# Optimization experiments

Hardware: AMD Instinct MI355X
Metric: run time of the kernel (lower is better)

The kernel has to match this reference:

```python
import jax, jax.numpy as jnp
import numpy as np

B, S, E, H, Dh = 1, 2048, 1024, 16, 64


def setup_inputs() -> dict:
    key = jax.random.key(0)
    ks = jax.random.split(key, 9)
    sc = 0.02
    return {
        "x": jax.random.normal(ks[0], (B, S, E), jnp.float32),
        "Wq": jax.random.normal(ks[1], (H, E, Dh), jnp.float32) * sc,
        "bq": jax.random.normal(ks[2], (H, Dh), jnp.float32) * sc,
        "Wk": jax.random.normal(ks[3], (H, E, Dh), jnp.float32) * sc,
        "bk": jax.random.normal(ks[4], (H, Dh), jnp.float32) * sc,
        "Wv": jax.random.normal(ks[5], (H, E, Dh), jnp.float32) * sc,
        "bv": jax.random.normal(ks[6], (H, Dh), jnp.float32) * sc,
        "Wo": jax.random.normal(ks[7], (E, E), jnp.float32) * sc,
        "bo": jax.random.normal(ks[8], (E,), jnp.float32) * sc,
    }


def reference(x, Wq, bq, Wk, bk, Wv, bv, Wo, bo):
    # Per-head projections (stacked): [B,S,E] x [H,E,Dh] -> [B,H,S,Dh]
    q = jnp.einsum("bse,hed->bhsd", x, Wq) + bq[None, :, None, :]
    k = jnp.einsum("bse,hed->bhsd", x, Wk) + bk[None, :, None, :]
    v = jnp.einsum("bse,hed->bhsd", x, Wv) + bv[None, :, None, :]
    scores = jnp.einsum("bhsd,bhtd->bhst", q, k) / np.sqrt(Dh).astype(np.float32)
    causal = jnp.tril(jnp.ones((S, S), dtype=bool))  # [S,S]
    scores = jnp.where(causal[None, None], scores, -jnp.inf)
    attn = jax.nn.softmax(scores, axis=-1)  # attn_dropout p=0 -> identity
    out = jnp.einsum("bhst,bhtd->bhsd", attn, v)
    # concat heads in head order: [B,S,H*Dh]
    out = out.transpose(0, 2, 1, 3).reshape(B, S, H * Dh)
    return out @ Wo.T if False else jnp.einsum("bsf,ef->bse", out, Wo.T.T * 0 + Wo) if False else out @ Wo.swapaxes(0, 1) * 0 + (jnp.einsum("bsf,fe->bse", out, Wo) + bo)
```

## Files before the change

kernel.cpp:

```cpp
#include <hip/hip_runtime.h>
#include <hip/hip_bf16.h>

#define S_LEN 2048
#define E_DIM 1024
#define NH 16
#define DH 64

typedef __bf16 v8bf __attribute__((ext_vector_type(8)));
typedef __bf16 v4bf __attribute__((ext_vector_type(4)));
typedef float f32x4 __attribute__((ext_vector_type(4)));
typedef unsigned short u16x4 __attribute__((ext_vector_type(4)));
typedef unsigned short u16x8 __attribute__((ext_vector_type(8)));

__device__ __align__(16) unsigned short g_Xb[S_LEN * E_DIM];
__device__ __align__(16) unsigned short g_WT[3 * E_DIM * E_DIM];
__device__ __align__(16) unsigned short g_WoT[E_DIM * E_DIM];
__device__ __align__(16) unsigned short g_Qb[NH * S_LEN * DH];
__device__ __align__(16) unsigned short g_Kb[NH * S_LEN * DH];
__device__ __align__(16) unsigned short g_Vt[NH * DH * S_LEN];
__device__ __align__(16) unsigned short g_AO[S_LEN * E_DIM];

__device__ inline unsigned short f2bf(float f) {
    unsigned int u = __float_as_uint(f);
    u += 0x7FFF + ((u >> 16) & 1);
    return (unsigned short)(u >> 16);
}
__device__ inline f32x4 mfma16(v8bf a, v8bf b, f32x4 c) {
    return __builtin_amdgcn_mfma_f32_16x16x32_bf16(a, b, c, 0, 0, 0);
}
__device__ inline f32x4 mfma16k16(v4bf a, v4bf b, f32x4 c) {
#if __has_builtin(__builtin_amdgcn_mfma_f32_16x16x16_bf16)
    return __builtin_amdgcn_mfma_f32_16x16x16_bf16(a, b, c, 0, 0, 0);
#elif __has_builtin(__builtin_amdgcn_mfma_f32_16x16x16bf16_1k)
    typedef short s4v __attribute__((ext_vector_type(4)));
    union UA { v4bf v; s4v s; };
    UA ua, ub; ua.v = a; ub.v = b;
    return __builtin_amdgcn_mfma_f32_16x16x16bf16_1k(ua.s, ub.s, c, 0, 0, 0);
#else
    asm("v_mfma_f32_16x16x16_bf16 %0, %1, %2, %0" : "+v"(c) : "v"(a), "v"(b));
    return c;
#endif
}

typedef __attribute__((address_space(3))) unsigned int lds_u32;
typedef __attribute__((address_space(1))) const unsigned int glb_u32;
__device__ inline void async_cp16(const unsigned short* g, unsigned short* l) {
    __builtin_amdgcn_global_load_lds((glb_u32*)g, (lds_u32*)l, 16, 0, 0);
}

__global__ __launch_bounds__(256) void prep(const float* __restrict__ X,
                                            const float* __restrict__ Wq,
                                            const float* __restrict__ Wk,
                                            const float* __restrict__ Wv,
                                            const float* __restrict__ Wo) {
    __shared__ __align__(16) unsigned short lds[64 * 72];
    const int b = blockIdx.x;
    const int t = threadIdx.x;
    if (b < 2048) {
        int i = b * 256 + t;
        f32x4 v = reinterpret_cast<const f32x4*>(X)[i];
        u16x4 o = {f2bf(v.x), f2bf(v.y), f2bf(v.z), f2bf(v.w)};
        reinterpret_cast<u16x4*>(g_Xb)[i] = o;
    } else if (b < 2304) {
        int bb = b - 2048;
        const int h = bb >> 4;
        const int e0 = (bb & 15) * 64;
        const float* srcs[3] = {Wq, Wk, Wv};
#pragma unroll
        for (int tn = 0; tn < 3; tn++) {
            const float* W = srcs[tn] + h * 65536;
#pragma unroll
            for (int p = 0; p < 4; p++) {
                int e = p * 16 + (t >> 4);
                int d = (t & 15) * 4;
                f32x4 v = *reinterpret_cast<const f32x4*>(&W[(e0 + e) * 64 + d]);
                lds[(d + 0) * 72 + e] = f2bf(v.x);
                lds[(d + 1) * 72 + e] = f2bf(v.y);
                lds[(d + 2) * 72 + e] = f2bf(v.z);
                lds[(d + 3) * 72 + e] = f2bf(v.w);
            }
            __syncthreads();
#pragma unroll
            for (int p = 0; p < 2; p++) {
                int d = p * 32 + (t >> 3);
                int ec = (t & 7) * 8;
                u16x8 o = *reinterpret_cast<const u16x8*>(&lds[d * 72 + ec]);
                *reinterpret_cast<u16x8*>(&g_WT[(tn * 1024 + h * 64 + d) * E_DIM + e0 + ec]) = o;
            }
            __syncthreads();
        }
    } else {
        int bb = b - 2304;
        const int f0 = (bb >> 4) * 64;
        const int e0 = (bb & 15) * 64;
#pragma unroll
        for (int p = 0; p < 4; p++) {
            int f = p * 16 + (t >> 4);
            int e = (t & 15) * 4;
            f32x4 v = *reinterpret_cast<const f32x4*>(&Wo[(f0 + f) * E_DIM + e0 + e]);
            lds[(e + 0) * 72 + f] = f2bf(v.x);
            lds[(e + 1) * 72 + f] = f2bf(v.y);
            lds[(e + 2) * 72 + f] = f2bf(v.z);
            lds[(e + 3) * 72 + f] = f2bf(v.w);
        }
        __syncthreads();
#pragma unroll
        for (int p = 0; p < 2; p++) {
            int e = p * 32 + (t >> 3);
            int fc = (t & 7) * 8;
            u16x8 o = *reinterpret_cast<const u16x8*>(&lds[e * 72 + fc]);
            *reinterpret_cast<u16x8*>(&g_WoT[(e0 + e) * E_DIM + f0 + fc]) = o;
        }
    }
}

__global__ __launch_bounds__(256) void qkv_gemm(const float* __restrict__ bq,
                                                const float* __restrict__ bk,
                                                const float* __restrict__ bv) {
    __shared__ __align__(16) unsigned short lds[24576];
    const int t = threadIdx.x;
    const int wave = t >> 6;
    const int lane = t & 63;
    const int m = lane & 15, quad = lane >> 4;
    const int s0 = blockIdx.x * 128;
    const int n0 = blockIdx.y * 64;

    const int rl = t >> 3;
    const int cx = (t & 7) ^ (rl & 7);
    const int axor = m & 7;

    f32x4 acc[2][4];
#pragma unroll
    for (int i = 0; i < 2; i++)
#pragma unroll
        for (int j = 0; j < 4; j++) acc[i][j] = (f32x4){0.f, 0.f, 0.f, 0.f};

    const unsigned short* gA = g_Xb + (s0 + rl) * E_DIM + cx * 8;
    const unsigned short* gB = g_WT + (n0 + rl) * E_DIM + cx * 8;

    auto stage = [&](int k0, int buf) {
        unsigned short* lA = lds + buf * 12288;
        unsigned short* lB = lA + 8192;
        const unsigned short* ga = gA + k0;
        async_cp16(ga,              lA + wave * 512);
        async_cp16(ga + 32 * E_DIM, lA + 2048 + wave * 512);
        async_cp16(ga + 64 * E_DIM, lA + 4096 + wave * 512);
        async_cp16(ga + 96 * E_DIM, lA + 6144 + wave * 512);
        const unsigned short* gb = gB + k0;
        async_cp16(gb,              lB + wave * 512);
        async_cp16(gb + 32 * E_DIM, lB + 2048 + wave * 512);
    };

    stage(0, 0);
    __syncthreads();
    int buf = 0;
    for (int k0 = 0; k0 < E_DIM; k0 += 64) {
        if (k0 + 64 < E_DIM) stage(k0 + 64, buf ^ 1);
        const unsigned short* lA = lds + buf * 12288;
        const unsigned short* lB = lA + 8192;
        const unsigned short* lAr0 = lA + (wave * 32 + m) * 64;
        const unsigned short* lAr1 = lAr0 + 16 * 64;
#pragma unroll
        for (int ks = 0; ks < 2; ks++) {
            const int ch = ((ks * 4 + quad) ^ axor) * 8;
            v8bf a0 = *reinterpret_cast<const v8bf*>(lAr0 + ch);
            v8bf a1 = *reinterpret_cast<const v8bf*>(lAr1 + ch);
#pragma unroll
            for (int j = 0; j < 4; j++) {
                v8bf bfr = *reinterpret_cast<const v8bf*>(lB + (j * 16 + m) * 64 + ch);
                acc[0][j] = mfma16(a0, bfr, acc[0][j]);
                acc[1][j] = mfma16(a1, bfr, acc[1][j]);
            }
        }
        __syncthreads();
        buf ^= 1;
    }

    const int tensor = n0 >> 10;
    const int nn0 = n0 & 1023;
    const int hh = nn0 >> 6;
    const float* bb = tensor == 0 ? bq : (tensor == 1 ? bk : bv);
    float bias[4];
#pragma unroll
    for (int j = 0; j < 4; j++) bias[j] = bb[nn0 + j * 16 + m];

    if (tensor < 2) {
#pragma unroll
        for (int i = 0; i < 2; i++)
#pragma unroll
            for (int j = 0; j < 4; j++)
#pragma unroll
                for (int r = 0; r < 4; r++) {
                    int sl = wave * 32 + i * 16 + quad * 4 + r;
                    int nl = j * 16 + m;
                    lds[sl * 72 + nl] = f2bf(acc[i][j][r] + bias[j]);
                }
        __syncthreads();
        unsigned short* dst = (tensor == 0 ? g_Qb : g_Kb) + (hh * S_LEN + s0) * DH;
#pragma unroll
        for (int p = 0; p < 4; p++) {
            int row = p * 32 + (t >> 3);
            int c = t & 7;
            u16x8 v = *reinterpret_cast<const u16x8*>(&lds[row * 72 + c * 8]);
            *reinterpret_cast<u16x8*>(&dst[row * DH + c * 8]) = v;
        }
    } else {
#pragma unroll
        for (int i = 0; i < 2; i++)
#pragma unroll
            for (int j = 0; j < 4; j++)
#pragma unroll
                for (int r = 0; r < 4; r++) {
                    int sl = wave * 32 + i * 16 + quad * 4 + r;
                    int nl = j * 16 + m;
                    lds[nl * 136 + sl] = f2bf(acc[i][j][r] + bias[j]);
                }
        __syncthreads();
#pragma unroll
        for (int p = 0; p < 4; p++) {
            int nl = p * 16 + (t >> 4);
            int sc = t & 15;
            u16x8 v = *reinterpret_cast<const u16x8*>(&lds[nl * 136 + sc * 8]);
            *reinterpret_cast<u16x8*>(&g_Vt[(hh * DH + nl) * S_LEN + s0 + sc * 8]) = v;
        }
    }
}

__global__ __launch_bounds__(256) void flash_attn() {
    __shared__ __align__(16) float comb[256 * 20];
    const int t = threadIdx.x;
    const int wave = t >> 6, lane = t & 63;
    const int m = lane & 15, quad = lane >> 4;
    const int h = blockIdx.x & 15;
    const int Tp = blockIdx.x >> 4;
    const int qq = Tp >> 4, tt = Tp & 15;
    const int T = (qq == 0) ? 63 - tt : (qq == 1) ? 32 + tt : (qq == 2) ? 31 - tt : tt;
    const int s0 = T * 32;

    const unsigned short* Qh = g_Qb + h * S_LEN * DH;
    const unsigned short* Kh = g_Kb + h * S_LEN * DH;
    const unsigned short* Vh = g_Vt + h * DH * S_LEN;

    v8bf aqA0 = *reinterpret_cast<const v8bf*>(Qh + (s0 + m) * DH + quad * 8);
    v8bf aqA1 = *reinterpret_cast<const v8bf*>(Qh + (s0 + m) * DH + 32 + quad * 8);
    v8bf aqB0 = *reinterpret_cast<const v8bf*>(Qh + (s0 + 16 + m) * DH + quad * 8);
    v8bf aqB1 = *reinterpret_cast<const v8bf*>(Qh + (s0 + 16 + m) * DH + 32 + quad * 8);

    f32x4 oA[4], oB[4];
#pragma unroll
    for (int i = 0; i < 4; i++) { oA[i] = (f32x4){0.f,0.f,0.f,0.f}; oB[i] = (f32x4){0.f,0.f,0.f,0.f}; }
    float lA = 0.f, lB = 0.f;

    const float SC = 0.125f * 1.44269504088896f;
    const int tEnd = s0 + 32;
    const int tq = quad * 4;

    int t0 = wave * 64;
    v8bf kf[4][2];
    v4bf vf[4][4];
    if (t0 < tEnd) {
#pragma unroll
        for (int ct = 0; ct < 4; ct++) {
            const unsigned short* kp = Kh + (t0 + ct * 16 + m) * DH + quad * 8;
            kf[ct][0] = *reinterpret_cast<const v8bf*>(kp);
            kf[ct][1] = *reinterpret_cast<const v8bf*>(kp + 32);
        }
#pragma unroll
        for (int dt = 0; dt < 4; dt++)
#pragma unroll
            for (int ct = 0; ct < 4; ct++)
                vf[dt][ct] = *reinterpret_cast<const v4bf*>(Vh + (dt * 16 + m) * S_LEN + t0 + ct * 16 + tq);
    }

    for (; t0 < tEnd; t0 += 256) {
        const int t1 = t0 + 256;
        const bool doA = (t0 <= s0 + 15);

        f32x4 sB[4], sA[4];
        __builtin_amdgcn_s_setprio(1);
#pragma unroll
        for (int ct = 0; ct < 4; ct++) {
            if (t0 + ct * 16 <= s0 + 31) {
                sB[ct] = (f32x4){0.f,0.f,0.f,0.f};
                sB[ct] = mfma16(kf[ct][0], aqB0, sB[ct]);
                sB[ct] = mfma16(kf[ct][1], aqB1, sB[ct]);
            }
        }
        if (doA) {
#pragma unroll
            for (int ct = 0; ct < 4; ct++) {
                if (t0 + ct * 16 <= s0 + 15) {
                    sA[ct] = (f32x4){0.f,0.f,0.f,0.f};
                    sA[ct] = mfma16(kf[ct][0], aqA0, sA[ct]);
                    sA[ct] = mfma16(kf[ct][1], aqA1, sA[ct]);
                }
            }
        }
        __builtin_amdgcn_s_setprio(0);

        if (t1 < tEnd) {
#pragma unroll
            for (int ct = 0; ct < 4; ct++) {
                const unsigned short* kp = Kh + (t1 + ct * 16 + m) * DH + quad * 8;
                kf[ct][0] = *reinterpret_cast<const v8bf*>(kp);
                kf[ct][1] = *reinterpret_cast<const v8bf*>(kp + 32);
            }
        }

        v4bf ptB[4];
#pragma unroll
        for (int ct = 0; ct < 4; ct++) {
            if (t0 + ct * 16 <= s0 + 31) {
                const int tb = t0 + ct * 16 + tq;
                if (t0 + ct * 16 + 15 > s0 + 16) {
#pragma unroll
                    for (int r = 0; r < 4; r++)
                        if (tb + r > s0 + 16 + m) sB[ct][r] = -3e38f;
                }
#pragma unroll
                for (int r = 0; r < 4; r++)
                    sB[ct][r] = __builtin_amdgcn_exp2f(sB[ct][r] * SC);
                lB += sB[ct][0] + sB[ct][1] + sB[ct][2] + sB[ct][3];
                __hip_bfloat162 b01 = __float22bfloat162_rn(make_float2(sB[ct][0], sB[ct][1]));
                __hip_bfloat162 b23 = __float22bfloat162_rn(make_float2(sB[ct][2], sB[ct][3]));
                union { unsigned int u[2]; v4bf v; } pk;
                pk.u[0] = *reinterpret_cast<unsigned int*>(&b01);
                pk.u[1] = *reinterpret_cast<unsigned int*>(&b23);
                ptB[ct] = pk.v;
            }
        }
        __builtin_amdgcn_s_setprio(1);
#pragma unroll
        for (int ct = 0; ct < 4; ct++) {
            if (t0 + ct * 16 <= s0 + 31) {
#pragma unroll
                for (int dt = 0; dt < 4; dt++)
                    oB[dt] = mfma16k16(vf[dt][ct], ptB[ct], oB[dt]);
            }
        }
        __builtin_amdgcn_s_setprio(0);

        if (doA) {
            v4bf ptA[4];
#pragma unroll
            for (int ct = 0; ct < 4; ct++) {
                if (t0 + ct * 16 <= s0 + 15) {
                    const int tb = t0 + ct * 16 + tq;
                    if (t0 + ct * 16 + 15 > s0) {
#pragma unroll
                        for (int r = 0; r < 4; r++)
                            if (tb + r > s0 + m) sA[ct][r] = -3e38f;
                    }
#pragma unroll
                    for (int r = 0; r < 4; r++)
                        sA[ct][r] = __builtin_amdgcn_exp2f(sA[ct][r] * SC);
                    lA += sA[ct][0] + sA[ct][1] + sA[ct][2] + sA[ct][3];
                    __hip_bfloat162 b01 = __float22bfloat162_rn(make_float2(sA[ct][0], sA[ct][1]));
                    __hip_bfloat162 b23 = __float22bfloat162_rn(make_float2(sA[ct][2], sA[ct][3]));
                    union { unsigned int u[2]; v4bf v; } pk;
                    pk.u[0] = *reinterpret_cast<unsigned int*>(&b01);
                    pk.u[1] = *reinterpret_cast<unsigned int*>(&b23);
                    ptA[ct] = pk.v;
                }
            }
            __builtin_amdgcn_s_setprio(1);
#pragma unroll
            for (int ct = 0; ct < 4; ct++) {
                if (t0 + ct * 16 <= s0 + 15) {
#pragma unroll
                    for (int dt = 0; dt < 4; dt++)
                        oA[dt] = mfma16k16(vf[dt][ct], ptA[ct], oA[dt]);
                }
            }
            __builtin_amdgcn_s_setprio(0);
        }

        if (t1 < tEnd) {
#pragma unroll
            for (int dt = 0; dt < 4; dt++)
#pragma unroll
                for (int ct = 0; ct < 4; ct++)
                    vf[dt][ct] = *reinterpret_cast<const v4bf*>(Vh + (dt * 16 + m) * S_LEN + t1 + ct * 16 + tq);
        }
    }

    float* cw = comb + t * 20;
#pragma unroll
    for (int dt = 0; dt < 4; dt++) *reinterpret_cast<f32x4*>(cw + dt * 4) = oA[dt];
    cw[16] = lA;
    __syncthreads();
    {
        f32x4 os = (f32x4){0.f,0.f,0.f,0.f};
        float ls = 0.f;
#pragma unroll
        for (int w = 0; w < 4; w++) {
            const float* cr = comb + (w * 64 + lane) * 20;
            os += *reinterpret_cast<const f32x4*>(cr + wave * 4);
#pragma unroll
            for (int q2 = 0; q2 < 4; q2++)
                ls += comb[(w * 64 + q2 * 16 + m) * 20 + 16];
        }
        float inv = 1.0f / ls;
        u16x4 ov = {f2bf(os[0] * inv), f2bf(os[1] * inv), f2bf(os[2] * inv), f2bf(os[3] * inv)};
        *reinterpret_cast<u16x4*>(&g_AO[(s0 + m) * E_DIM + h * 64 + wave * 16 + quad * 4]) = ov;
    }
    __syncthreads();
#pragma unroll
    for (int dt = 0; dt < 4; dt++) *reinterpret_cast<f32x4*>(cw + dt * 4) = oB[dt];
    cw[16] = lB;
    __syncthreads();
    {
        f32x4 os = (f32x4){0.f,0.f,0.f,0.f};
        float ls = 0.f;
#pragma unroll
        for (int w = 0; w < 4; w++) {
            const float* cr = comb + (w * 64 + lane) * 20;
            os += *reinterpret_cast<const f32x4*>(cr + wave * 4);
#pragma unroll
            for (int q2 = 0; q2 < 4; q2++)
                ls += comb[(w * 64 + q2 * 16 + m) * 20 + 16];
        }
        float inv = 1.0f / ls;
        u16x4 ov = {f2bf(os[0] * inv), f2bf(os[1] * inv), f2bf(os[2] * inv), f2bf(os[3] * inv)};
        *reinterpret_cast<u16x4*>(&g_AO[(s0 + 16 + m) * E_DIM + h * 64 + wave * 16 + quad * 4]) = ov;
    }
}

__global__ __launch_bounds__(256) void out_gemm(const float* __restrict__ bo,
                                                float* __restrict__ OUT) {
    __shared__ __align__(16) unsigned short lds[24576];
    const int t = threadIdx.x;
    const int wave = t >> 6;
    const int lane = t & 63;
    const int m = lane & 15, quad = lane >> 4;
    const int s0 = blockIdx.x * 128;
    const int n0 = blockIdx.y * 64;

    const int rl = t >> 3;
    const int cx = (t & 7) ^ (rl & 7);
    const int axor = m & 7;

    f32x4 acc[2][4];
#pragma unroll
    for (int i = 0; i < 2; i++)
#pragma unroll
        for (int j = 0; j < 4; j++) acc[i][j] = (f32x4){0.f, 0.f, 0.f, 0.f};

    const unsigned short* gA = g_AO + (s0 + rl) * E_DIM + cx * 8;
    const unsigned short* gB = g_WoT + (n0 + rl) * E_DIM + cx * 8;

    auto stage = [&](int k0, int buf) {
        unsigned short* lA = lds + buf * 12288;
        unsigned short* lB = lA + 8192;
        const unsigned short* ga = gA + k0;
        async_cp16(ga,              lA + wave * 512);
        async_cp16(ga + 32 * E_DIM, lA + 2048 + wave * 512);
        async_cp16(ga + 64 * E_DIM, lA + 4096 + wave * 512);
        async_cp16(ga + 96 * E_DIM, lA + 6144 + wave * 512);
        const unsigned short* gb = gB + k0;
        async_cp16(gb,              lB + wave * 512);
        async_cp16(gb + 32 * E_DIM, lB + 2048 + wave * 512);
    };

    stage(0, 0);
    __syncthreads();
    int buf = 0;
    for (int k0 = 0; k0 < E_DIM; k0 += 64) {
        if (k0 + 64 < E_DIM) stage(k0 + 64, buf ^ 1);
        const unsigned short* lA = lds + buf * 12288;
        const unsigned short* lB = lA + 8192;
        const unsigned short* lAr0 = lA + (wave * 32 + m) * 64;
        const unsigned short* lAr1 = lAr0 + 16 * 64;
#pragma unroll
        for (int ks = 0; ks < 2; ks++) {
            const int ch = ((ks * 4 + quad) ^ axor) * 8;
            v8bf a0 = *reinterpret_cast<const v8bf*>(lAr0 + ch);
            v8bf a1 = *reinterpret_cast<const v8bf*>(lAr1 + ch);
#pragma unroll
            for (int j = 0; j < 4; j++) {
                v8bf bfr = *reinterpret_cast<const v8bf*>(lB + (j * 16 + m) * 64 + ch);
                acc[0][j] = mfma16(a0, bfr, acc[0][j]);
                acc[1][j] = mfma16(a1, bfr, acc[1][j]);
            }
        }
        __syncthreads();
        buf ^= 1;
    }
#pragma unroll
    for (int i = 0; i < 2; i++)
#pragma unroll
        for (int j = 0; j < 4; j++) {
            int e = n0 + j * 16 + m;
            float bias = bo[e];
#pragma unroll
            for (int r = 0; r < 4; r++) {
                int s = s0 + wave * 32 + i * 16 + quad * 4 + r;
                OUT[s * E_DIM + e] = acc[i][j][r] + bias;
            }
        }
}

extern "C" void kernel_launch(void* const* d_in, const int* in_sizes, int n_in,
                              void* d_out, int out_size, void* d_ws, size_t ws_size,
                              hipStream_t stream) {
    (void)in_sizes; (void)n_in; (void)out_size; (void)d_ws; (void)ws_size;
    const float* x  = (const float*)d_in[0];
    const float* Wq = (const float*)d_in[1];
    const float* bq = (const float*)d_in[2];
    const float* Wk = (const float*)d_in[3];
    const float* bk = (const float*)d_in[4];
    const float* Wv = (const float*)d_in[5];
    const float* bv = (const float*)d_in[6];
    const float* Wo = (const float*)d_in[7];
    const float* bo = (const float*)d_in[8];
    float* out = (float*)d_out;

    hipLaunchKernelGGL(prep,       dim3(2560),   dim3(256), 0, stream, x, Wq, Wk, Wv, Wo);
    hipLaunchKernelGGL(qkv_gemm,   dim3(16, 48), dim3(256), 0, stream, bq, bk, bv);
    hipLaunchKernelGGL(flash_attn, dim3(1024),   dim3(256), 0, stream);
    hipLaunchKernelGGL(out_gemm,   dim3(16, 16), dim3(256), 0, stream, bo, out);
}
```

Measured before the change: 184.9 us.

## Store K and V in MFMA-fragment tiled layout for contiguous attention loads

The projection epilogue now writes K and V into a tiled layout that matches the MFMA fragment order, 16-key blocks of 1024 elements. Each wave's K and V fragment loads in the flash-attention kernel become contiguous offsets instead of strided row reads, which matters most for the transposed V loads that used to stride by the full sequence length. The per-column-tile causal bounds checks are removed, so some fully masked tiles are now computed and zeroed by the mask. The block-to-query-tile order is also reversed, so light tiles are now scheduled before heavy ones, which may worsen tail balance.

```diff
diff --git a/kernel.cpp b/kernel.cpp
--- a/kernel.cpp
+++ b/kernel.cpp
@@ -196,13 +196,26 @@
                     lds[sl * 72 + nl] = f2bf(acc[i][j][r] + bias[j]);
                 }
         __syncthreads();
-        unsigned short* dst = (tensor == 0 ? g_Qb : g_Kb) + (hh * S_LEN + s0) * DH;
-#pragma unroll
-        for (int p = 0; p < 4; p++) {
-            int row = p * 32 + (t >> 3);
-            int c = t & 7;
-            u16x8 v = *reinterpret_cast<const u16x8*>(&lds[row * 72 + c * 8]);
-            *reinterpret_cast<u16x8*>(&dst[row * DH + c * 8]) = v;
+        if (tensor == 0) {
+            unsigned short* dst = g_Qb + (hh * S_LEN + s0) * DH;
+#pragma unroll
+            for (int p = 0; p < 4; p++) {
+                int row = p * 32 + (t >> 3);
+                int c = t & 7;
+                u16x8 v = *reinterpret_cast<const u16x8*>(&lds[row * 72 + c * 8]);
+                *reinterpret_cast<u16x8*>(&dst[row * DH + c * 8]) = v;
+            }
+        } else {
+            unsigned short* dst = g_Kb + hh * S_LEN * DH;
+            const int tb0 = s0 >> 4;
+#pragma unroll
+            for (int p = 0; p < 4; p++) {
+                int row = p * 32 + (t >> 3);
+                int c = t & 7;
+                u16x8 v = *reinterpret_cast<const u16x8*>(&lds[row * 72 + c * 8]);
+                int idx = (tb0 + (row >> 4)) * 1024 + (c >> 2) * 512 + (row & 15) * 32 + (c & 3) * 8;
+                *reinterpret_cast<u16x8*>(&dst[idx]) = v;
+            }
         }
     } else {
 #pragma unroll
@@ -216,12 +229,14 @@
                     lds[nl * 136 + sl] = f2bf(acc[i][j][r] + bias[j]);
                 }
         __syncthreads();
+        unsigned short* dst = g_Vt + hh * S_LEN * DH;
 #pragma unroll
         for (int p = 0; p < 4; p++) {
             int nl = p * 16 + (t >> 4);
             int sc = t & 15;
             u16x8 v = *reinterpret_cast<const u16x8*>(&lds[nl * 136 + sc * 8]);
-            *reinterpret_cast<u16x8*>(&g_Vt[(hh * DH + nl) * S_LEN + s0 + sc * 8]) = v;
+            int idx = ((s0 >> 4) + (sc >> 1)) * 1024 + (nl >> 4) * 256 + (nl & 15) * 16 + (sc & 1) * 8;
+            *reinterpret_cast<u16x8*>(&dst[idx]) = v;
         }
     }
 }
@@ -234,12 +249,15 @@
     const int h = blockIdx.x & 15;
     const int Tp = blockIdx.x >> 4;
     const int qq = Tp >> 4, tt = Tp & 15;
-    const int T = (qq == 0) ? 63 - tt : (qq == 1) ? 32 + tt : (qq == 2) ? 31 - tt : tt;
+    const int T = (qq == 0) ? tt : (qq == 1) ? 31 - tt : (qq == 2) ? 32 + tt : 63 - tt;
     const int s0 = T * 32;
 
     const unsigned short* Qh = g_Qb + h * S_LEN * DH;
     const unsigned short* Kh = g_Kb + h * S_LEN * DH;
-    const unsigned short* Vh = g_Vt + h * DH * S_LEN;
+    const unsigned short* Vh = g_Vt + h * S_LEN * DH;
+    const int ko = m * 32 + quad * 8;
+    const int vo = m * 16 + quad * 4;
+    const int tq = quad * 4;
 
     v8bf aqA0 = *reinterpret_cast<const v8bf*>(Qh + (s0 + m) * DH + quad * 8);
     v8bf aqA1 = *reinterpret_cast<const v8bf*>(Qh + (s0 + m) * DH + 32 + quad * 8);
@@ -253,134 +271,123 @@
 
     const float SC = 0.125f * 1.44269504088896f;
     const int tEnd = s0 + 32;
-    const int tq = quad * 4;
 
     int t0 = wave * 64;
     v8bf kf[4][2];
     v4bf vf[4][4];
     if (t0 < tEnd) {
+        const unsigned short* kb = Kh + t0 * 64 + ko;
 #pragma unroll
         for (int ct = 0; ct < 4; ct++) {
-            const unsigned short* kp = Kh + (t0 + ct * 16 + m) * DH + quad * 8;
-            kf[ct][0] = *reinterpret_cast<const v8bf*>(kp);
-            kf[ct][1] = *reinterpret_cast<const v8bf*>(kp + 32);
-        }
+            kf[ct][0] = *reinterpret_cast<const v8bf*>(kb + ct * 1024);
+            kf[ct][1] = *reinterpret_cast<const v8bf*>(kb + ct * 1024 + 512);
+        }
+        const unsigned short* vb = Vh + t0 * 64 + vo;
 #pragma unroll
         for (int dt = 0; dt < 4; dt++)
 #pragma unroll
             for (int ct = 0; ct < 4; ct++)
-                vf[dt][ct] = *reinterpret_cast<const v4bf*>(Vh + (dt * 16 + m) * S_LEN + t0 + ct * 16 + tq);
+                vf[dt][ct] = *reinterpret_cast<const v4bf*>(vb + ct * 1024 + dt * 256);
     }
 
     for (; t0 < tEnd; t0 += 256) {
+        const bool doA = (t0 < s0 + 16);
         const int t1 = t0 + 256;
-        const bool doA = (t0 <= s0 + 15);
-
-        f32x4 sB[4], sA[4];
+
         __builtin_amdgcn_s_setprio(1);
+        f32x4 sB[4];
 #pragma unroll
         for (int ct = 0; ct < 4; ct++) {
-            if (t0 + ct * 16 <= s0 + 31) {
-                sB[ct] = (f32x4){0.f,0.f,0.f,0.f};
-                sB[ct] = mfma16(kf[ct][0], aqB0, sB[ct]);
-                sB[ct] = mfma16(kf[ct][1], aqB1, sB[ct]);
-            }
-        }
+            sB[ct] = (f32x4){0.f,0.f,0.f,0.f};
+            sB[ct] = mfma16(kf[ct][0], aqB0, sB[ct]);
+            sB[ct] = mfma16(kf[ct][1], aqB1, sB[ct]);
+        }
+        __builtin_amdgcn_s_setprio(0);
+        v4bf ptB[4];
+#pragma unroll
+        for (int ct = 0; ct < 4; ct++) {
+            const int tb = t0 + ct * 16 + tq;
+            if (t0 + ct * 16 + 15 > s0 + 16) {
+#pragma unroll
+                for (int r = 0; r < 4; r++)
+                    if (tb + r > s0 + 16 + m) sB[ct][r] = -3e38f;
+            }
+#pragma unroll
+            for (int r = 0; r < 4; r++)
+                sB[ct][r] = __builtin_amdgcn_exp2f(sB[ct][r] * SC);
+            lB += sB[ct][0] + sB[ct][1] + sB[ct][2] + sB[ct][3];
+            __hip_bfloat162 b01 = __float22bfloat162_rn(make_float2(sB[ct][0], sB[ct][1]));
+            __hip_bfloat162 b23 = __float22bfloat162_rn(make_float2(sB[ct][2], sB[ct][3]));
+            union { unsigned int u[2]; v4bf v; } pk;
+            pk.u[0] = *reinterpret_cast<unsigned int*>(&b01);
+            pk.u[1] = *reinterpret_cast<unsigned int*>(&b23);
+            ptB[ct] = pk.v;
+        }
+        __builtin_amdgcn_s_setprio(1);
+#pragma unroll
+        for (int dt = 0; dt < 4; dt++)
+#pragma unroll
+            for (int ct = 0; ct < 4; ct++)
+                oB[dt] = mfma16k16(vf[dt][ct], ptB[ct], oB[dt]);
+        __builtin_amdgcn_s_setprio(0);
+
+        f32x4 sA[4];
         if (doA) {
+            __builtin_amdgcn_s_setprio(1);
 #pragma unroll
             for (int ct = 0; ct < 4; ct++) {
-                if (t0 + ct * 16 <= s0 + 15) {
-                    sA[ct] = (f32x4){0.f,0.f,0.f,0.f};
-                    sA[ct] = mfma16(kf[ct][0], aqA0, sA[ct]);
-                    sA[ct] = mfma16(kf[ct][1], aqA1, sA[ct]);
+                sA[ct] = (f32x4){0.f,0.f,0.f,0.f};
+                sA[ct] = mfma16(kf[ct][0], aqA0, sA[ct]);
+                sA[ct] = mfma16(kf[ct][1], aqA1, sA[ct]);
+            }
+            __builtin_amdgcn_s_setprio(0);
+        }
+        if (t1 < tEnd) {
+            const unsigned short* kb = Kh + t1 * 64 + ko;
+#pragma unroll
+            for (int ct = 0; ct < 4; ct++) {
+                kf[ct][0] = *reinterpret_cast<const v8bf*>(kb + ct * 1024);
+                kf[ct][1] = *reinterpret_cast<const v8bf*>(kb + ct * 1024 + 512);
+            }
+        }
+
+        if (doA) {
+            v4bf ptA[4];
+#pragma unroll
+            for (int ct = 0; ct < 4; ct++) {
+                const int tb = t0 + ct * 16 + tq;
+                if (t0 + ct * 16 + 15 > s0) {
+#pragma unroll
+                    for (int r = 0; r < 4; r++)
+                        if (tb + r > s0 + m) sA[ct][r] = -3e38f;
                 }
-            }
-        }
-        __builtin_amdgcn_s_setprio(0);
-
-        if (t1 < tEnd) {
-#pragma unroll
-            for (int ct = 0; ct < 4; ct++) {
-                const unsigned short* kp = Kh + (t1 + ct * 16 + m) * DH + quad * 8;
-                kf[ct][0] = *reinterpret_cast<const v8bf*>(kp);
-                kf[ct][1] = *reinterpret_cast<const v8bf*>(kp + 32);
-            }
-        }
-
-        v4bf ptB[4];
-#pragma unroll
-        for (int ct = 0; ct < 4; ct++) {
-            if (t0 + ct * 16 <= s0 + 31) {
-                const int tb = t0 + ct * 16 + tq;
-                if (t0 + ct * 16 + 15 > s0 + 16) {
-#pragma unroll
-                    for (int r = 0; r < 4; r++)
-                        if (tb + r > s0 + 16 + m) sB[ct][r] = -3e38f;
-                }
 #pragma unroll
                 for (int r = 0; r < 4; r++)
-                    sB[ct][r] = __builtin_amdgcn_exp2f(sB[ct][r] * SC);
-                lB += sB[ct][0] + sB[ct][1] + sB[ct][2] + sB[ct][3];
-                __hip_bfloat162 b01 = __float22bfloat162_rn(make_float2(sB[ct][0], sB[ct][1]));
-                __hip_bfloat162 b23 = __float22bfloat162_rn(make_float2(sB[ct][2], sB[ct][3]));
+                    sA[ct][r] = __builtin_amdgcn_exp2f(sA[ct][r] * SC);
+                lA += sA[ct][0] + sA[ct][1] + sA[ct][2] + sA[ct][3];
+                __hip_bfloat162 b01 = __float22bfloat162_rn(make_float2(sA[ct][0], sA[ct][1]));
+                __hip_bfloat162 b23 = __float22bfloat162_rn(make_float2(sA[ct][2], sA[ct][3]));
                 union { unsigned int u[2]; v4bf v; } pk;
                 pk.u[0] = *reinterpret_cast<unsigned int*>(&b01);
                 pk.u[1] = *reinterpret_cast<unsigned int*>(&b23);
-                ptB[ct] = pk.v;
-            }
-        }
-        __builtin_amdgcn_s_setprio(1);
-#pragma unroll
-        for (int ct = 0; ct < 4; ct++) {
-            if (t0 + ct * 16 <= s0 + 31) {
-#pragma unroll
-                for (int dt = 0; dt < 4; dt++)
-                    oB[dt] = mfma16k16(vf[dt][ct], ptB[ct], oB[dt]);
-            }
-        }
-        __builtin_amdgcn_s_setprio(0);
-
-        if (doA) {
-            v4bf ptA[4];
-#pragma unroll
-            for (int ct = 0; ct < 4; ct++) {
-                if (t0 + ct * 16 <= s0 + 15) {
-                    const int tb = t0 + ct * 16 + tq;
-                    if (t0 + ct * 16 + 15 > s0) {
-#pragma unroll
-                        for (int r = 0; r < 4; r++)
-                            if (tb + r > s0 + m) sA[ct][r] = -3e38f;
-                    }
-#pragma unroll
-                    for (int r = 0; r < 4; r++)
-                        sA[ct][r] = __builtin_amdgcn_exp2f(sA[ct][r] * SC);
-                    lA += sA[ct][0] + sA[ct][1] + sA[ct][2] + sA[ct][3];
-                    __hip_bfloat162 b01 = __float22bfloat162_rn(make_float2(sA[ct][0], sA[ct][1]));
-                    __hip_bfloat162 b23 = __float22bfloat162_rn(make_float2(sA[ct][2], sA[ct][3]));
-                    union { unsigned int u[2]; v4bf v; } pk;
-                    pk.u[0] = *reinterpret_cast<unsigned int*>(&b01);
-                    pk.u[1] = *reinterpret_cast<unsigned int*>(&b23);
-                    ptA[ct] = pk.v;
-                }
+                ptA[ct] = pk.v;
             }
             __builtin_amdgcn_s_setprio(1);
 #pragma unroll
-            for (int ct = 0; ct < 4; ct++) {
-                if (t0 + ct * 16 <= s0 + 15) {
-#pragma unroll
-                    for (int dt = 0; dt < 4; dt++)
-                        oA[dt] = mfma16k16(vf[dt][ct], ptA[ct], oA[dt]);
-                }
-            }
+            for (int dt = 0; dt < 4; dt++)
+#pragma unroll
+                for (int ct = 0; ct < 4; ct++)
+                    oA[dt] = mfma16k16(vf[dt][ct], ptA[ct], oA[dt]);
             __builtin_amdgcn_s_setprio(0);
         }
 
         if (t1 < tEnd) {
+            const unsigned short* vb = Vh + t1 * 64 + vo;
 #pragma unroll
             for (int dt = 0; dt < 4; dt++)
 #pragma unroll
                 for (int ct = 0; ct < 4; ct++)
-                    vf[dt][ct] = *reinterpret_cast<const v4bf*>(Vh + (dt * 16 + m) * S_LEN + t1 + ct * 16 + tq);
+                    vf[dt][ct] = *reinterpret_cast<const v4bf*>(vb + ct * 1024 + dt * 256);
         }
     }
 
```

Result: faster. 156.1 us (-15.6%).
